# Optimization experiments

Measured on AMD Instinct MI355X. Metric: run time of the kernel, lower is better.

## Reference

```python
import jax, jax.numpy as jnp
import numpy as np

B, STEP, H, N_ENC = 256, 32, 512, 60
PD, LD, NB, NTYPE, NPLAYER = 32, 32, 6, 11, 35


def _parity_masks(S):
    # Static relation-11/12 edge masks from update_adjacency_matrix (step is a Python int).
    m11 = np.zeros((S, S), dtype=bool)
    m12 = np.zeros((S, S), dtype=bool)
    for row in range(S):
        ni = row // 2
        if row % 2 == 0:
            c = (ni + 1) * 2
            if c <= S - 1:
                (m11 if ni % 2 == 0 else m12)[row, c] = True
                (m11 if ni % 2 == 0 else m12)[c, row] = True
        else:
            c = (ni + 1) * 2 + 1
            if c <= S - 1:
                (m12 if ni % 2 == 0 else m11)[row, c] = True
                (m12 if ni % 2 == 0 else m11)[c, row] = True
    return jnp.asarray(m11), jnp.asarray(m12)


def update_adjacency(adj, step, shot_type_predict=False):
    b = adj.shape[0]
    S = step * 2
    new = jnp.zeros((b, 13, S, S), dtype=adj.dtype).at[:, :, :S - 2, :S - 2].set(adj)
    m11, m12 = _parity_masks(S)
    new = new.at[:, 11].set(jnp.where(m11, 1, new[:, 11]))
    new = new.at[:, 12].set(jnp.where(m12, 1, new[:, 12]))
    if shot_type_predict:
        idx = (step - 1) * 2 if step % 2 == 0 else (step - 1) * 2 + 1
        new = new.at[:, :, idx, :].set(0).at[:, :, :, idx].set(0)
    return new


def rgcn(node, adj, layer_params):
    # adj: (B,13,N,N) int; slice off relation 0 -> 12 relations. Dropout is eval-mode identity.
    adj_f = adj[:, 1:].astype(node.dtype)  # (B,12,N,N)
    x = node
    n_layers = len(layer_params)
    for i, (basis, comb, w_self) in enumerate(layer_params):
        act = jax.nn.sigmoid if i == n_layers - 1 else jax.nn.relu
        W = jnp.einsum('rb,bij->rij', comb, basis)            # (12,H,H)
        msg = jnp.einsum('brnm,bmh->brnh', adj_f, x)          # (B,12,N,H)
        x = act(jnp.einsum('brnh,rhk->bnk', msg, W) + x @ w_self.T)
    return x


def setup_inputs() -> dict:
    key = jax.random.key(0)
    ks = jax.random.split(key, 20)
    s = 0.05
    return {
        'player': jax.random.randint(ks[0], (B, 2), 0, NPLAYER, dtype=jnp.int32),
        'step': STEP,
        'encode_node_embedding': jax.random.normal(ks[1], (B, N_ENC, H), jnp.float32),
        'adjacency_matrix': jax.random.randint(ks[2], (B, 13, (STEP - 1) * 2, (STEP - 1) * 2), 0, 2, dtype=jnp.int32),
        'player_A_x': jax.random.uniform(ks[3], (B, 1), jnp.float32),
        'player_A_y': jax.random.uniform(ks[4], (B, 1), jnp.float32),
        'player_B_x': jax.random.uniform(ks[5], (B, 1), jnp.float32),
        'player_B_y': jax.random.uniform(ks[6], (B, 1), jnp.float32),
        'emb_table': jax.random.normal(ks[7], (NPLAYER, PD), jnp.float32) * s,
        'coord_W': jax.random.normal(ks[8], (LD, 2), jnp.float32) * s,
        'coord_b': jnp.zeros((LD,), jnp.float32),
        'in_W': jax.random.normal(ks[9], (H, PD + LD), jnp.float32) * s,
        'in_b': jnp.zeros((H,), jnp.float32),
        'basis0': jax.random.normal(ks[10], (NB, H, H), jnp.float32) * s,
        'comb0': jax.random.normal(ks[11], (12, NB), jnp.float32) * s,
        'self0': jax.random.normal(ks[12], (H, H), jnp.float32) * s,
        'basis1': jax.random.normal(ks[13], (NB, H, H), jnp.float32) * s,
        'comb1': jax.random.normal(ks[14], (12, NB), jnp.float32) * s,
        'self1': jax.random.normal(ks[15], (H, H), jnp.float32) * s,
        'type_W': jax.random.normal(ks[16], (NTYPE, 2 * H), jnp.float32) * s,
        'type_b': jnp.zeros((NTYPE,), jnp.float32),
    }


def reference(player, step, encode_node_embedding, adjacency_matrix,
              player_A_x, player_A_y, player_B_x, player_B_y,
              emb_table, coord_W, coord_b, in_W, in_b,
              basis0, comb0, self0, basis1, comb1, self1, type_W, type_b):
    b = player.shape[0]
    layers = [(basis0, comb0, self0), (basis1, comb1, self1)]

    coord_A = jnp.stack([player_A_x, player_A_y], axis=2)   # (B,1,2)
    coord_B = jnp.stack([player_B_x, player_B_y], axis=2)   # (B,1,2)
    coords = jnp.stack([coord_A, coord_B], axis=2).reshape(b, -1, 2)  # (B,2,2)
    loc = jax.nn.relu(coords @ coord_W.T + coord_b)          # (B,2,LD)
    pemb = emb_table[player]                                 # (B,2,PD)
    initial = jnp.concatenate([loc, pemb], axis=-1) @ in_W.T + in_b  # (B,2,H)

    # first=False branch: current coords == prev coords, so model_input == initial
    mi = jnp.concatenate([encode_node_embedding, initial], axis=1)   # (B,62,H)
    tmp = rgcn(mi, adjacency_matrix, layers)
    passed = jnp.concatenate([encode_node_embedding[:, :-2], tmp[:, -4:]], axis=1)  # (B,62,H)

    tmp_adj = update_adjacency(adjacency_matrix, step, shot_type_predict=True)  # (B,13,64,64)
    mi2 = jnp.concatenate([passed, initial], axis=1)         # (B,64,H)
    drop = (step - 1) * 2 if step % 2 == 0 else (step - 1) * 2 + 1
    keep = np.delete(np.arange(step * 2), drop)
    mi2 = mi2[:, keep]
    tmp_adj = tmp_adj[:, :, keep][:, :, :, keep]
    tmp2 = rgcn(mi2, tmp_adj, layers)                        # (B,63,H)

    pad = jnp.zeros((b, tmp2.shape[1] + 1, tmp2.shape[2]), tmp2.dtype)
    if step % 2 == 0:
        pad = pad.at[:, :-2].set(tmp2[:, :-1]).at[:, -1].set(tmp2[:, -1])
    else:
        pad = pad.at[:, :-1].set(tmp2)
    stp = jnp.concatenate([passed[:, :-2], pad[:, -4:]], axis=1)  # (B,64,H)
    if step % 2 == 0:
        black = stp[:, (step - 1) * 2 + 1]
        white = stp[:, (step - 2) * 2]
    else:
        black = stp[:, (step - 2) * 2 + 1]
        white = stp[:, (step - 1) * 2]
    logits = jnp.concatenate([black, white], axis=-1) @ type_W.T + type_b
    return logits
```

## Files before the change

### kernel.cpp

```cpp
#include <hip/hip_runtime.h>
#include <hip/hip_bf16.h>

typedef unsigned short u16;
typedef unsigned long long u64;
typedef __attribute__((ext_vector_type(4))) short short4v;
typedef __attribute__((ext_vector_type(8))) short short8;
typedef __attribute__((ext_vector_type(4))) float floatx4;

__device__ __forceinline__ u16 f2bf(float f) {
    union { float f; unsigned u; } v; v.f = f;
    unsigned r = v.u + 0x7FFF + ((v.u >> 16) & 1);
    return (u16)(r >> 16);
}

__global__ void k_wcat(const float* __restrict__ basis, const float* __restrict__ selfW,
                       u16* __restrict__ wf) {
    int bi = blockIdx.x, t = threadIdx.x;
    int kr = t >> 7;
    int nb = (t & 127) * 4;
    for (int it = 0; it < 4; ++it) {
        int k = bi * 8 + it * 2 + kr;
        float v0, v1, v2, v3;
        if (k < 3072) {
            int q = k >> 9, h = k & 511;
            const float4 bz = *(const float4*)(basis + ((size_t)(q * 512 + h)) * 512 + nb);
            v0 = bz.x; v1 = bz.y; v2 = bz.z; v3 = bz.w;
        } else {
            int kk = k - 3072;
            v0 = selfW[(size_t)(nb + 0) * 512 + kk];
            v1 = selfW[(size_t)(nb + 1) * 512 + kk];
            v2 = selfW[(size_t)(nb + 2) * 512 + kk];
            v3 = selfW[(size_t)(nb + 3) * 512 + kk];
        }
        float vv[4] = {v0, v1, v2, v3};
        for (int i = 0; i < 4; ++i) {
            int n = nb + i;
            wf[(size_t)(k >> 5) * 16384 + (n >> 4) * 512 + ((k >> 3) & 3) * 128 + (n & 15) * 8 + (k & 7)] = f2bf(vv[i]);
        }
    }
}

#define AQ_SETSTRIDE (256UL * 6 * 4096)
__global__ void k_adjq(const int* __restrict__ A, const float* __restrict__ comb0,
                       const float* __restrict__ comb1, u16* __restrict__ aq, int variant) {
    int b = blockIdx.x, t = threadIdx.x;
    __shared__ u64 sm[12][64];
    __shared__ float cmb[2][12][6];
    if (t < 72) { cmb[0][t / 6][t % 6] = comb0[t]; cmb[1][t / 6][t % 6] = comb1[t]; }
    for (int rr = 0; rr < 3; ++rr) {
        int r = rr * 4 + (t >> 6), n = t & 63;
        const int* Ab = A + (size_t)(b * 13 + (r + 1)) * 62 * 62;
        u64 m = 0;
        if (variant == 0) {
            if (n < 62)
                for (int mm = 0; mm < 62; ++mm)
                    if (Ab[n * 62 + mm]) m |= 1ull << mm;
        } else {
            if (n < 63) {
                int oi = (n == 62) ? 63 : n;
                for (int mm = 0; mm < 63; ++mm) {
                    int oj = (mm == 62) ? 63 : mm;
                    int val = (oi < 62 && oj < 62) ? (Ab[oi * 62 + oj] ? 1 : 0) : 0;
                    int lo = (oi < oj) ? oi : oj, hi = (oi < oj) ? oj : oi;
                    if (hi == lo + 2) {
                        int p = (lo >> 1) & 1;
                        int chp = ((lo & 1) == 0) ? (p ? 12 : 11) : (p ? 11 : 12);
                        if (r + 1 == chp) val = 1;
                    }
                    if (val) m |= 1ull << mm;
                }
            }
        }
        sm[r][n] = m;
    }
    __syncthreads();
    for (int ii = 0; ii < 16; ++ii) {
        int pos = ii * 256 + t;
        int f = pos >> 9, lane = (pos >> 3) & 63, j = pos & 7;
        int row = ((f >> 1) << 4) + (lane & 15);
        int mb  = ((f & 1) << 5) + ((lane >> 4) << 3) + j;
        float bits[12];
        #pragma unroll
        for (int r = 0; r < 12; ++r) bits[r] = (float)((sm[r][row] >> mb) & 1ull);
        #pragma unroll
        for (int s = 0; s < 2; ++s)
            #pragma unroll
            for (int q = 0; q < 6; ++q) {
                float v = 0.f;
                #pragma unroll
                for (int r = 0; r < 12; ++r) v += bits[r] * cmb[s][r][q];
                aq[(size_t)s * AQ_SETSTRIDE + ((size_t)b * 6 + q) * 4096 + pos] = f2bf(v);
            }
    }
}

__global__ void k_prep(const int* __restrict__ player,
                       const float* __restrict__ pAx, const float* __restrict__ pAy,
                       const float* __restrict__ pBx, const float* __restrict__ pBy,
                       const float* __restrict__ emb, const float* __restrict__ cW,
                       const float* __restrict__ cb, const float* __restrict__ inW,
                       const float* __restrict__ inb,
                       u16* __restrict__ mi1, u16* __restrict__ mi2) {
    int b = blockIdx.x, t = threadIdx.x;
    __shared__ float feat[2][64];
    if (t < 64) {
        int j = t >> 5, d = t & 31;
        float X = j ? pBx[b] : pAx[b];
        float Y = j ? pBy[b] : pAy[b];
        feat[j][d] = fmaxf(cW[d * 2] * X + cW[d * 2 + 1] * Y + cb[d], 0.f);
        feat[j][32 + d] = emb[player[b * 2 + j] * 32 + d];
    }
    __syncthreads();
    for (int h = t; h < 512; h += 256) {
        float a0 = inb[h], a1 = inb[h];
        const float* wrow = inW + h * 64;
        #pragma unroll
        for (int d = 0; d < 64; ++d) {
            float wv = wrow[d];
            a0 += wv * feat[0][d];
            a1 += wv * feat[1][d];
        }
        u16 v0 = f2bf(a0), v1 = f2bf(a1);
        size_t base = (size_t)b * 64 * 512;
        mi1[base + 60 * 512 + h] = v0;
        mi1[base + 61 * 512 + h] = v1;
        mi1[base + 62 * 512 + h] = 0;
        mi1[base + 63 * 512 + h] = 0;
        mi2[base + 62 * 512 + h] = v1;
        mi2[base + 63 * 512 + h] = 0;
    }
}

__global__ void k_cast(const float* __restrict__ enc, u16* __restrict__ mi1, u16* __restrict__ mi2) {
    long long e = ((long long)blockIdx.x * 256 + threadIdx.x) * 8;
    if (e >= 256LL * 60 * 512) return;
    int b = (int)(e / (60 * 512));
    int rm = (int)(e % (60 * 512));
    int n = rm / 512, h = rm % 512;
    for (int i = 0; i < 8; ++i) {
        u16 v = f2bf(enc[e + i]);
        mi1[((size_t)b * 64 + n) * 512 + h + i] = v;
        if (n < 58) mi2[((size_t)b * 64 + n) * 512 + h + i] = v;
    }
}

__global__ __launch_bounds__(512, 2)
void k_layer(const u16* __restrict__ x, const u16* __restrict__ aq,
             const u16* __restrict__ wc, u16* __restrict__ out) {
    int b = blockIdx.x;
    int t = threadIdx.x, lane = t & 63, w = t >> 6;
    int l15 = lane & 15, lq = lane >> 4;
    const int TS = 520;
    __shared__ __align__(16) u16 T[64 * 520];

    const u16* xb_base = x + (size_t)b * 64 * 512;
    short8 xb[8];
    #pragma unroll
    for (int nt = 0; nt < 4; ++nt)
        #pragma unroll
        for (int kh = 0; kh < 2; ++kh) {
            int h = (w * 4 + nt) * 16 + l15;
            int j0 = kh * 32 + lq * 8;
            short8 v;
            #pragma unroll
            for (int jj = 0; jj < 8; ++jj)
                v[jj] = (short)xb_base[(size_t)(j0 + jj) * 512 + h];
            xb[nt * 2 + kh] = v;
        }

    floatx4 acc[16];
    #pragma unroll
    for (int i = 0; i < 16; ++i) acc[i] = (floatx4)(0.f);

    const u16* aqb   = aq + (size_t)b * 6 * 4096 + (size_t)lane * 8;
    const u16* wbase = wc + (size_t)lane * 8;

    for (int q = 0; q < 6; ++q) {
        __syncthreads();
        for (int i = 0; i < 4; ++i) {
            short8 a0 = *(const short8*)(aqb + (size_t)q * 4096 + (i * 2 + 0) * 512);
            short8 a1 = *(const short8*)(aqb + (size_t)q * 4096 + (i * 2 + 1) * 512);
            #pragma unroll
            for (int nt = 0; nt < 4; ++nt) {
                floatx4 tz = (floatx4)(0.f);
                tz = __builtin_amdgcn_mfma_f32_16x16x32_bf16(a0, xb[nt * 2 + 0], tz, 0, 0, 0);
                tz = __builtin_amdgcn_mfma_f32_16x16x32_bf16(a1, xb[nt * 2 + 1], tz, 0, 0, 0);
                int hcol = (w * 4 + nt) * 16 + l15;
                int mrow = i * 16 + lq * 4;
                #pragma unroll
                for (int reg = 0; reg < 4; ++reg)
                    T[(mrow + reg) * TS + hcol] = f2bf(tz[reg]);
            }
        }
        __syncthreads();
        for (int ks = 0; ks < 16; ++ks) {
            short8 af[4], bf[4];
            #pragma unroll
            for (int i = 0; i < 4; ++i)
                af[i] = *(const short8*)&T[(i * 16 + l15) * TS + ks * 32 + lq * 8];
            #pragma unroll
            for (int nt = 0; nt < 4; ++nt)
                bf[nt] = *(const short8*)(wbase + (size_t)(q * 16 + ks) * 16384 + (size_t)(w * 4 + nt) * 512);
            #pragma unroll
            for (int i = 0; i < 4; ++i)
                #pragma unroll
                for (int nt = 0; nt < 4; ++nt)
                    acc[i * 4 + nt] = __builtin_amdgcn_mfma_f32_16x16x32_bf16(af[i], bf[nt], acc[i * 4 + nt], 0, 0, 0);
        }
    }
    for (int ks = 0; ks < 16; ++ks) {
        short8 af[4], bf[4];
        #pragma unroll
        for (int i = 0; i < 4; ++i)
            af[i] = *(const short8*)(xb_base + (size_t)(i * 16 + l15) * 512 + ks * 32 + lq * 8);
        #pragma unroll
        for (int nt = 0; nt < 4; ++nt)
            bf[nt] = *(const short8*)(wbase + (size_t)(96 + ks) * 16384 + (size_t)(w * 4 + nt) * 512);
        #pragma unroll
        for (int i = 0; i < 4; ++i)
            #pragma unroll
            for (int nt = 0; nt < 4; ++nt)
                acc[i * 4 + nt] = __builtin_amdgcn_mfma_f32_16x16x32_bf16(af[i], bf[nt], acc[i * 4 + nt], 0, 0, 0);
    }
    #pragma unroll
    for (int i = 0; i < 4; ++i)
        #pragma unroll
        for (int nt = 0; nt < 4; ++nt) {
            int n = (w * 4 + nt) * 16 + l15;
            int m0 = i * 16 + lq * 4;
            #pragma unroll
            for (int reg = 0; reg < 4; ++reg)
                out[((size_t)b * 64 + m0 + reg) * 512 + n] = f2bf(fmaxf(acc[i * 4 + nt][reg], 0.f));
        }
}

__global__ __launch_bounds__(512, 2)
void k_layer_last(const u16* __restrict__ x, const u16* __restrict__ aq,
                  const u16* __restrict__ wc, int mode,
                  u16* __restrict__ o16, float* __restrict__ o32) {
    int b = blockIdx.x;
    int t = threadIdx.x, lane = t & 63, w = t >> 6;
    int l15 = lane & 15, lq = lane >> 4;
    const int TS = 520;
    __shared__ __align__(16) u16 T[16 * 520];

    const u16* xb_base = x + (size_t)b * 64 * 512;
    short8 xb[8];
    #pragma unroll
    for (int nt = 0; nt < 4; ++nt)
        #pragma unroll
        for (int kh = 0; kh < 2; ++kh) {
            int h = (w * 4 + nt) * 16 + l15;
            int j0 = kh * 32 + lq * 8;
            short8 v;
            #pragma unroll
            for (int jj = 0; jj < 8; ++jj)
                v[jj] = (short)xb_base[(size_t)(j0 + jj) * 512 + h];
            xb[nt * 2 + kh] = v;
        }

    floatx4 acc[4];
    #pragma unroll
    for (int i = 0; i < 4; ++i) acc[i] = (floatx4)(0.f);

    const u16* aqb   = aq + (size_t)b * 6 * 4096 + (size_t)lane * 8;
    const u16* wbase = wc + (size_t)lane * 8;

    for (int q = 0; q < 6; ++q) {
        __syncthreads();
        {
            short8 a0 = *(const short8*)(aqb + (size_t)q * 4096 + 6 * 512);
            short8 a1 = *(const short8*)(aqb + (size_t)q * 4096 + 7 * 512);
            #pragma unroll
            for (int nt = 0; nt < 4; ++nt) {
                floatx4 tz = (floatx4)(0.f);
                tz = __builtin_amdgcn_mfma_f32_16x16x32_bf16(a0, xb[nt * 2 + 0], tz, 0, 0, 0);
                tz = __builtin_amdgcn_mfma_f32_16x16x32_bf16(a1, xb[nt * 2 + 1], tz, 0, 0, 0);
                int hcol = (w * 4 + nt) * 16 + l15;
                int mrow = lq * 4;
                #pragma unroll
                for (int reg = 0; reg < 4; ++reg)
                    T[(mrow + reg) * TS + hcol] = f2bf(tz[reg]);
            }
        }
        __syncthreads();
        for (int ks = 0; ks < 16; ++ks) {
            short8 af = *(const short8*)&T[l15 * TS + ks * 32 + lq * 8];
            #pragma unroll
            for (int nt = 0; nt < 4; ++nt) {
                short8 bf = *(const short8*)(wbase + (size_t)(q * 16 + ks) * 16384 + (size_t)(w * 4 + nt) * 512);
                acc[nt] = __builtin_amdgcn_mfma_f32_16x16x32_bf16(af, bf, acc[nt], 0, 0, 0);
            }
        }
    }
    for (int ks = 0; ks < 16; ++ks) {
        short8 af = *(const short8*)(xb_base + (size_t)(48 + l15) * 512 + ks * 32 + lq * 8);
        #pragma unroll
        for (int nt = 0; nt < 4; ++nt) {
            short8 bf = *(const short8*)(wbase + (size_t)(96 + ks) * 16384 + (size_t)(w * 4 + nt) * 512);
            acc[nt] = __builtin_amdgcn_mfma_f32_16x16x32_bf16(af, bf, acc[nt], 0, 0, 0);
        }
    }
    #pragma unroll
    for (int nt = 0; nt < 4; ++nt) {
        int n = (w * 4 + nt) * 16 + l15;
        #pragma unroll
        for (int reg = 0; reg < 4; ++reg) {
            int m = 48 + lq * 4 + reg;
            float v = acc[nt][reg];
            if (mode == 1) {
                if (m >= 58 && m <= 61)
                    o16[((size_t)b * 64 + m) * 512 + n] = f2bf(1.f / (1.f + __expf(-v)));
            } else {
                if (m == 60 || m == 62) {
                    int slot = (m == 60) ? (b * 2) : (b * 2 + 1);
                    o32[(size_t)slot * 512 + n] = 1.f / (1.f + __expf(-v));
                }
            }
        }
    }
}

__global__ void k_final(const float* __restrict__ t2, const float* __restrict__ tW,
                        const float* __restrict__ tb, float* __restrict__ outp) {
    int b = blockIdx.x, l = threadIdx.x;
    float a[11];
    #pragma unroll
    for (int j = 0; j < 11; ++j) a[j] = 0.f;
    for (int it = 0; it < 16; ++it) {
        int h = it * 64 + l;
        float c = (h < 512) ? t2[(b * 2 + 1) * 512 + h] : t2[(b * 2 + 0) * 512 + (h - 512)];
        #pragma unroll
        for (int j = 0; j < 11; ++j) a[j] += c * tW[j * 1024 + h];
    }
    #pragma unroll
    for (int j = 0; j < 11; ++j) {
        float v = a[j];
        for (int off = 32; off > 0; off >>= 1) v += __shfl_down(v, off, 64);
        if (l == 0) outp[b * 11 + j] = v + tb[j];
    }
}

extern "C" void kernel_launch(void* const* d_in, const int* in_sizes, int n_in,
                              void* d_out, int out_size, void* d_ws, size_t ws_size,
                              hipStream_t stream) {
    const int*   player = (const int*)d_in[0];
    const float* enc    = (const float*)d_in[2];
    const int*   adjm   = (const int*)d_in[3];
    const float* pAx    = (const float*)d_in[4];
    const float* pAy    = (const float*)d_in[5];
    const float* pBx    = (const float*)d_in[6];
    const float* pBy    = (const float*)d_in[7];
    const float* emb    = (const float*)d_in[8];
    const float* cW     = (const float*)d_in[9];
    const float* cb     = (const float*)d_in[10];
    const float* inW    = (const float*)d_in[11];
    const float* inb    = (const float*)d_in[12];
    const float* basis0 = (const float*)d_in[13];
    const float* comb0  = (const float*)d_in[14];
    const float* self0  = (const float*)d_in[15];
    const float* basis1 = (const float*)d_in[16];
    const float* comb1  = (const float*)d_in[17];
    const float* self1  = (const float*)d_in[18];
    const float* typeW  = (const float*)d_in[19];
    const float* typeb  = (const float*)d_in[20];

    char* ws = (char*)d_ws;
    size_t off = 0;
    auto alloc = [&](size_t bytes) -> void* {
        void* p = ws + off;
        off = (off + bytes + 255) & ~(size_t)255;
        return p;
    };
    u16* mi1   = (u16*)alloc(256UL * 64 * 512 * 2);
    u16* mi2   = (u16*)alloc(256UL * 64 * 512 * 2);
    u16* x12   = (u16*)alloc(256UL * 64 * 512 * 2);
    u16* aqbuf = (u16*)alloc(2UL * AQ_SETSTRIDE * 2);
    u16* wcat0 = (u16*)alloc(3584UL * 512 * 2);
    u16* wcat1 = (u16*)alloc(3584UL * 512 * 2);
    u16* x12b  = mi1;
    float* t2  = (float*)x12;
    u16* aq0   = aqbuf;
    u16* aq1   = aqbuf + AQ_SETSTRIDE;

    k_wcat<<<448, 256, 0, stream>>>(basis0, self0, wcat0);
    k_wcat<<<448, 256, 0, stream>>>(basis1, self1, wcat1);
    k_adjq<<<256, 256, 0, stream>>>(adjm, comb0, comb1, aqbuf, 0);
    k_prep<<<256, 256, 0, stream>>>(player, pAx, pAy, pBx, pBy, emb, cW, cb, inW, inb, mi1, mi2);
    k_cast<<<3840, 256, 0, stream>>>(enc, mi1, mi2);

    k_layer<<<256, 512, 0, stream>>>(mi1, aq0, wcat0, x12);
    k_layer_last<<<256, 512, 0, stream>>>(x12, aq1, wcat1, 1, mi2, nullptr);
    k_adjq<<<256, 256, 0, stream>>>(adjm, comb0, comb1, aqbuf, 1);
    k_layer<<<256, 512, 0, stream>>>(mi2, aq0, wcat0, x12b);
    k_layer_last<<<256, 512, 0, stream>>>(x12b, aq1, wcat1, 2, nullptr, t2);

    k_final<<<256, 64, 0, stream>>>(t2, typeW, typeb, (float*)d_out);
}
```

Measured before the change: 706.0 us.

## Split adjacency quantization into coalesced ballot mask kernel and parallel expansion

Replaces the per-batch k_adjq kernel with two kernels. k_masks builds both adjacency bitmask variants in one pass, one wavefront per (batch, relation), reading rows coalesced across lanes and packing bits with __ballot. k_aqexp then expands these masks into bf16 combined-adjacency fragments over 8x more blocks. The old kernel did serial strided per-thread loads and had too few blocks. The change adds a small mask buffer in the workspace and one extra launch.

```diff
diff --git a/kernel.cpp b/kernel.cpp
--- a/kernel.cpp
+++ b/kernel.cpp
@@ -40,48 +40,54 @@
     }
 }
 
+__global__ void k_masks(const int* __restrict__ A, u64* __restrict__ m0, u64* __restrict__ m1) {
+    int bi = blockIdx.x;
+    int b = bi / 12, r = bi % 12;
+    const int* Ab = A + (size_t)(b * 13 + (r + 1)) * 62 * 62;
+    int lane = threadIdx.x;
+    u64 my0 = 0, my1 = 0;
+    for (int n = 0; n < 64; ++n) {
+        int raw = 0;
+        if (n < 62 && lane < 62) raw = (Ab[n * 62 + lane] != 0) ? 1 : 0;
+        u64 b0 = __ballot(raw != 0);
+        int v1 = 0;
+        if (n < 63 && lane < 63) {
+            int oi = (n == 62) ? 63 : n;
+            int oj = (lane == 62) ? 63 : lane;
+            v1 = (oi < 62 && oj < 62) ? raw : 0;
+            int lo = (oi < oj) ? oi : oj, hi = (oi < oj) ? oj : oi;
+            if (hi == lo + 2) {
+                int p = (lo >> 1) & 1;
+                int chp = ((lo & 1) == 0) ? (p ? 12 : 11) : (p ? 11 : 12);
+                if (r + 1 == chp) v1 = 1;
+            }
+        }
+        u64 b1 = __ballot(v1 != 0);
+        if (lane == n) { my0 = b0; my1 = b1; }
+    }
+    m0[(size_t)bi * 64 + lane] = my0;
+    m1[(size_t)bi * 64 + lane] = my1;
+}
+
 #define AQ_SETSTRIDE (256UL * 6 * 4096)
-__global__ void k_adjq(const int* __restrict__ A, const float* __restrict__ comb0,
-                       const float* __restrict__ comb1, u16* __restrict__ aq, int variant) {
-    int b = blockIdx.x, t = threadIdx.x;
-    __shared__ u64 sm[12][64];
+__global__ void k_aqexp(const u64* __restrict__ msk, const float* __restrict__ comb0,
+                        const float* __restrict__ comb1, u16* __restrict__ aq) {
+    int b = blockIdx.x >> 3, sp = blockIdx.x & 7;
+    int t = threadIdx.x;
+    __shared__ u64 sm[12 * 64];
     __shared__ float cmb[2][12][6];
     if (t < 72) { cmb[0][t / 6][t % 6] = comb0[t]; cmb[1][t / 6][t % 6] = comb1[t]; }
-    for (int rr = 0; rr < 3; ++rr) {
-        int r = rr * 4 + (t >> 6), n = t & 63;
-        const int* Ab = A + (size_t)(b * 13 + (r + 1)) * 62 * 62;
-        u64 m = 0;
-        if (variant == 0) {
-            if (n < 62)
-                for (int mm = 0; mm < 62; ++mm)
-                    if (Ab[n * 62 + mm]) m |= 1ull << mm;
-        } else {
-            if (n < 63) {
-                int oi = (n == 62) ? 63 : n;
-                for (int mm = 0; mm < 63; ++mm) {
-                    int oj = (mm == 62) ? 63 : mm;
-                    int val = (oi < 62 && oj < 62) ? (Ab[oi * 62 + oj] ? 1 : 0) : 0;
-                    int lo = (oi < oj) ? oi : oj, hi = (oi < oj) ? oj : oi;
-                    if (hi == lo + 2) {
-                        int p = (lo >> 1) & 1;
-                        int chp = ((lo & 1) == 0) ? (p ? 12 : 11) : (p ? 11 : 12);
-                        if (r + 1 == chp) val = 1;
-                    }
-                    if (val) m |= 1ull << mm;
-                }
-            }
-        }
-        sm[r][n] = m;
-    }
+    for (int i = t; i < 768; i += 256) sm[i] = msk[(size_t)b * 768 + i];
     __syncthreads();
-    for (int ii = 0; ii < 16; ++ii) {
-        int pos = ii * 256 + t;
+    #pragma unroll
+    for (int ii2 = 0; ii2 < 2; ++ii2) {
+        int pos = (sp * 2 + ii2) * 256 + t;
         int f = pos >> 9, lane = (pos >> 3) & 63, j = pos & 7;
         int row = ((f >> 1) << 4) + (lane & 15);
         int mb  = ((f & 1) << 5) + ((lane >> 4) << 3) + j;
         float bits[12];
         #pragma unroll
-        for (int r = 0; r < 12; ++r) bits[r] = (float)((sm[r][row] >> mb) & 1ull);
+        for (int r = 0; r < 12; ++r) bits[r] = (float)((sm[r * 64 + row] >> mb) & 1ull);
         #pragma unroll
         for (int s = 0; s < 2; ++s)
             #pragma unroll
@@ -378,6 +384,8 @@
     u16* aqbuf = (u16*)alloc(2UL * AQ_SETSTRIDE * 2);
     u16* wcat0 = (u16*)alloc(3584UL * 512 * 2);
     u16* wcat1 = (u16*)alloc(3584UL * 512 * 2);
+    u64* mm0   = (u64*)alloc(256UL * 12 * 64 * 8);
+    u64* mm1   = (u64*)alloc(256UL * 12 * 64 * 8);
     u16* x12b  = mi1;
     float* t2  = (float*)x12;
     u16* aq0   = aqbuf;
@@ -385,13 +393,14 @@
 
     k_wcat<<<448, 256, 0, stream>>>(basis0, self0, wcat0);
     k_wcat<<<448, 256, 0, stream>>>(basis1, self1, wcat1);
-    k_adjq<<<256, 256, 0, stream>>>(adjm, comb0, comb1, aqbuf, 0);
+    k_masks<<<3072, 64, 0, stream>>>(adjm, mm0, mm1);
+    k_aqexp<<<2048, 256, 0, stream>>>(mm0, comb0, comb1, aqbuf);
     k_prep<<<256, 256, 0, stream>>>(player, pAx, pAy, pBx, pBy, emb, cW, cb, inW, inb, mi1, mi2);
     k_cast<<<3840, 256, 0, stream>>>(enc, mi1, mi2);
 
     k_layer<<<256, 512, 0, stream>>>(mi1, aq0, wcat0, x12);
     k_layer_last<<<256, 512, 0, stream>>>(x12, aq1, wcat1, 1, mi2, nullptr);
-    k_adjq<<<256, 256, 0, stream>>>(adjm, comb0, comb1, aqbuf, 1);
+    k_aqexp<<<2048, 256, 0, stream>>>(mm1, comb0, comb1, aqbuf);
     k_layer<<<256, 512, 0, stream>>>(mi2, aq0, wcat0, x12b);
     k_layer_last<<<256, 512, 0, stream>>>(x12b, aq1, wcat1, 2, nullptr, t2);
 
```

After: 624.4 us. -11.6%, faster.
